# Kernel tuning notes

Measured on AMD Instinct MI355X. Metric: run time of the kernel, lower is better.

The kernel has to match this reference:

```python
import jax, jax.numpy as jnp
import numpy as np


def setup_inputs() -> dict:
    key = jax.random.key(0)
    k_in, k_w, k_s = jax.random.split(key, 3)
    B, S, D_IN, D_OUT = 4, 2048, 4096, 4096
    inp = jax.random.normal(k_in, (B, S, D_IN), dtype=jnp.float32)
    # int8 weight in [-128, 127], stored as int32 carrier then cast to int8
    int8_weight = jax.random.randint(k_w, (D_OUT, D_IN), -128, 128, dtype=jnp.int32).astype(jnp.int8)
    scale = jax.random.normal(k_s, (D_OUT,), dtype=jnp.float32)  # per-output-channel scale
    bias = jnp.zeros((1, D_OUT), dtype=jnp.float32)
    return {"input": inp, "int8_weight": int8_weight, "scale": scale, "bias": bias}


def reference(input, int8_weight, scale, bias):
    # w8a16 forward: cast int8 weight to activation dtype, linear, per-channel scale, bias
    w = int8_weight.astype(input.dtype)              # [out, in]
    out = jnp.einsum('bsi,oi->bso', input, w)        # F.linear
    out = out * scale                                # per-out-channel scale, broadcasts over [B,S]
    out = out + bias                                 # bias is [1, out], broadcasts
    return out
```

## Files before the change

### kernel.cpp

```cpp
#include <hip/hip_runtime.h>
#include <hip/hip_bf16.h>
#include <stdint.h>

typedef __attribute__((ext_vector_type(4))) int v4i;

#define BM 128
#define BN 128
#define BK 64

__device__ inline void load_lds16(const void* g, void* l) {
  __builtin_amdgcn_global_load_lds(
      (const __attribute__((address_space(1))) uint32_t*)g,
      (__attribute__((address_space(3))) uint32_t*)l, 16, 0, 0);
}

__global__ void detect_i32_kernel(const uint32_t* __restrict__ w, int n_words,
                                  int* __restrict__ flag) {
  __shared__ int s_ok;
  if (threadIdx.x == 0) s_ok = 1;
  __syncthreads();
  int ok = 1;
  for (int i = threadIdx.x; i < n_words; i += blockDim.x) {
    uint32_t v = w[i];
    uint32_t expect = (v & 0x80u) ? 0xFFFFFFu : 0u;
    if ((v >> 8) != expect) ok = 0;
  }
  if (!ok) s_ok = 0;
  __syncthreads();
  if (threadIdx.x == 0) *flag = s_ok;
}

__global__ __launch_bounds__(256)
void quant_a_kernel(const float* __restrict__ in, int8_t* __restrict__ out,
                    float* __restrict__ rscale, int K) {
  const int row = blockIdx.x;
  const int tid = threadIdx.x;
  const float4* p = (const float4*)(in + (size_t)row * K);
  float4 v[4];
  float amax = 0.f;
#pragma unroll
  for (int j = 0; j < 4; ++j) {
    v[j] = p[tid * 4 + j];
    amax = fmaxf(amax, fmaxf(fmaxf(fabsf(v[j].x), fabsf(v[j].y)),
                             fmaxf(fabsf(v[j].z), fabsf(v[j].w))));
  }
#pragma unroll
  for (int off = 32; off > 0; off >>= 1)
    amax = fmaxf(amax, __shfl_down(amax, off));
  __shared__ float s_part[4];
  __shared__ float s_inv, s_step;
  if ((tid & 63) == 0) s_part[tid >> 6] = amax;
  __syncthreads();
  if (tid == 0) {
    float m = fmaxf(fmaxf(s_part[0], s_part[1]), fmaxf(s_part[2], s_part[3]));
    s_inv  = (m > 0.f) ? 127.f / m : 0.f;
    s_step = (m > 0.f) ? m / 127.f : 0.f;
    rscale[row] = s_step;
  }
  __syncthreads();
  const float inv = s_inv;
  float f[16];
#pragma unroll
  for (int j = 0; j < 4; ++j) {
    f[4 * j]     = v[j].x; f[4 * j + 1] = v[j].y;
    f[4 * j + 2] = v[j].z; f[4 * j + 3] = v[j].w;
  }
  uint32_t w[4];
#pragma unroll
  for (int j = 0; j < 4; ++j) {
    uint32_t b = 0;
#pragma unroll
    for (int t = 0; t < 4; ++t) {
      int q = (int)rintf(f[4 * j + t] * inv);
      q = q > 127 ? 127 : (q < -127 ? -127 : q);
      b |= ((uint32_t)q & 0xffu) << (8 * t);
    }
    w[j] = b;
  }
  ((uint4*)(out + (size_t)row * K))[tid] = make_uint4(w[0], w[1], w[2], w[3]);
}

__global__ void repack_w_kernel(const void* __restrict__ in, int8_t* __restrict__ out,
                                int n16, const int* __restrict__ flag) {
  int i = blockIdx.x * blockDim.x + threadIdx.x;
  if (i >= n16) return;
  if (*flag) {
    uint32_t w[4];
#pragma unroll
    for (int j = 0; j < 4; ++j) {
      int4 a = ((const int4*)in)[4 * i + j];
      w[j] = ((uint32_t)a.x & 0xffu) | (((uint32_t)a.y & 0xffu) << 8) |
             (((uint32_t)a.z & 0xffu) << 16) | (((uint32_t)a.w & 0xffu) << 24);
    }
    ((uint4*)out)[i] = make_uint4(w[0], w[1], w[2], w[3]);
  } else {
    ((int4*)out)[i] = ((const int4*)in)[i];
  }
}

__global__ __launch_bounds__(256, 4)
void gemm_i8_epi(const int8_t* __restrict__ A, const int8_t* __restrict__ B,
                 const float* __restrict__ ascale, const float* __restrict__ scale,
                 const float* __restrict__ bias, float* __restrict__ C,
                 int Mdim, int Ndim, int Kdim) {
  __shared__ int8_t sA[BM * BK];
  __shared__ int8_t sB[BN * BK];
  __shared__ float sAs[BM];

  const int tid  = threadIdx.x;
  const int lane = tid & 63;
  const int wave = tid >> 6;
  const int wm = (wave >> 1) * 64;
  const int wn = (wave & 1) * 64;
  const int bm = blockIdx.y, bn = blockIdx.x;

  if (tid < BM) sAs[tid] = ascale[bm * BM + tid];

  const int srow = tid >> 2;
  const int scol = ((tid & 3) ^ (srow & 3)) * 16;
  const int8_t* gA = A + (size_t)(bm * BM + srow) * Kdim + scol;
  const int8_t* gB = B + (size_t)(bn * BN + srow) * Kdim + scol;

  const int frow = lane & 15;
  const int g    = lane >> 4;
  const int cpos = (g ^ (frow & 3)) * 16;

  v4i acc[4][4];
#pragma unroll
  for (int mi = 0; mi < 4; ++mi)
#pragma unroll
    for (int ni = 0; ni < 4; ++ni)
      acc[mi][ni] = (v4i){0, 0, 0, 0};

  for (int k0 = 0; k0 < Kdim; k0 += BK) {
    load_lds16(gA + k0,                       &sA[tid * 16]);
    load_lds16(gA + (size_t)64 * Kdim + k0,   &sA[4096 + tid * 16]);
    load_lds16(gB + k0,                       &sB[tid * 16]);
    load_lds16(gB + (size_t)64 * Kdim + k0,   &sB[4096 + tid * 16]);
    __syncthreads();

    v4i af[4], bf[4];
#pragma unroll
    for (int mi = 0; mi < 4; ++mi)
      af[mi] = *(const v4i*)&sA[(wm + frow + mi * 16) * BK + cpos];
#pragma unroll
    for (int ni = 0; ni < 4; ++ni)
      bf[ni] = *(const v4i*)&sB[(wn + frow + ni * 16) * BK + cpos];
#pragma unroll
    for (int mi = 0; mi < 4; ++mi)
#pragma unroll
      for (int ni = 0; ni < 4; ++ni)
        acc[mi][ni] = __builtin_amdgcn_mfma_i32_16x16x64_i8(
            af[mi], bf[ni], acc[mi][ni], 0, 0, 0);
    __syncthreads();
  }

  const int col0 = bn * BN + wn + (lane & 15);
  const int row0 = bm * BM + wm + (lane >> 4) * 4;
  const int lrow0 = wm + (lane >> 4) * 4;
#pragma unroll
  for (int ni = 0; ni < 4; ++ni) {
    int col = col0 + ni * 16;
    float sc = scale[col];
    float bs = bias[col];
#pragma unroll
    for (int mi = 0; mi < 4; ++mi) {
      int row = row0 + mi * 16;
#pragma unroll
      for (int r = 0; r < 4; ++r)
        C[(size_t)(row + r) * Ndim + col] =
            (float)acc[mi][ni][r] * sAs[lrow0 + mi * 16 + r] * sc + bs;
    }
  }
}

__global__ void naive_kernel(const float* __restrict__ A, const int* __restrict__ W,
                             const float* __restrict__ scale, const float* __restrict__ bias,
                             float* __restrict__ C, int Mdim, int Ndim, int Kdim) {
  int idx = blockIdx.x * blockDim.x + threadIdx.x;
  if (idx >= Mdim * Ndim) return;
  int row = idx / Ndim, col = idx % Ndim;
  const float* a = A + (size_t)row * Kdim;
  const int* w = W + (size_t)col * Kdim;
  float s = 0.f;
  for (int k = 0; k < Kdim; ++k) s += a[k] * (float)w[k];
  C[idx] = s * scale[col] + bias[col];
}

extern "C" void kernel_launch(void* const* d_in, const int* in_sizes, int n_in,
                              void* d_out, int out_size, void* d_ws, size_t ws_size,
                              hipStream_t stream) {
  const float* inp   = (const float*)d_in[0];
  const void*  w_raw = d_in[1];
  const float* scale = (const float*)d_in[2];
  const float* bias  = (const float*)d_in[3];
  float* out = (float*)d_out;

  const int N = in_sizes[2];
  const int K = in_sizes[1] / N;
  const int M = in_sizes[0] / K;

  size_t needA = (size_t)M * K;
  size_t needW = (size_t)N * K;
  size_t needS = (size_t)M * sizeof(float);
  size_t need  = needA + needW + needS + 16;
  if (ws_size < need) {
    int total = M * N;
    naive_kernel<<<(total + 255) / 256, 256, 0, stream>>>(
        inp, (const int*)w_raw, scale, bias, out, M, N, K);
    return;
  }

  int8_t* Aq = (int8_t*)d_ws;
  int8_t* Wq = Aq + needA;
  float* ascale = (float*)(Wq + needW);
  int* flag = (int*)(ascale + M);

  detect_i32_kernel<<<1, 256, 0, stream>>>((const uint32_t*)w_raw, 4096, flag);

  quant_a_kernel<<<M, 256, 0, stream>>>(inp, Aq, ascale, K);

  int nW16 = (N * K) / 16;
  repack_w_kernel<<<(nW16 + 255) / 256, 256, 0, stream>>>(w_raw, Wq, nW16, flag);

  dim3 grid(N / BN, M / BM);
  gemm_i8_epi<<<grid, 256, 0, stream>>>(Aq, Wq, ascale, scale, bias, out, M, N, K);
}
```

Measured before the change: 434.3 us.

## Replace int8 GEMM with 256x256 double-buffered 8-phase pipelined kernel

The GEMM moves from 128x128 single-buffered tiles to 256x256 tiles with 512 threads. It double-buffers 128-wide K slices in 128KB of LDS and interleaves the global-to-LDS loads with the MFMA phases, using barriers and setprio. It also adds an XCD-aware block swizzle, and rewrites quant_a and repack_w with coalesced 4-byte accesses per thread. The aim is to hide load latency and raise reuse per tile, at the cost of lower occupancy and shape restrictions that fall back to the naive kernel.

Result: faster. 392.2 us (-9.7%).

```diff
diff --git a/kernel.cpp b/kernel.cpp
--- a/kernel.cpp
+++ b/kernel.cpp
@@ -1,12 +1,7 @@
 #include <hip/hip_runtime.h>
-#include <hip/hip_bf16.h>
 #include <stdint.h>
 
 typedef __attribute__((ext_vector_type(4))) int v4i;
-
-#define BM 128
-#define BN 128
-#define BK 64
 
 __device__ inline void load_lds16(const void* g, void* l) {
   __builtin_amdgcn_global_load_lds(
@@ -36,142 +31,188 @@
   const int row = blockIdx.x;
   const int tid = threadIdx.x;
   const float4* p = (const float4*)(in + (size_t)row * K);
+  const int nf4 = K >> 2;
   float4 v[4];
   float amax = 0.f;
 #pragma unroll
   for (int j = 0; j < 4; ++j) {
-    v[j] = p[tid * 4 + j];
+    v[j] = p[tid + 256 * j];
     amax = fmaxf(amax, fmaxf(fmaxf(fabsf(v[j].x), fabsf(v[j].y)),
                              fmaxf(fabsf(v[j].z), fabsf(v[j].w))));
   }
+  (void)nf4;
 #pragma unroll
   for (int off = 32; off > 0; off >>= 1)
     amax = fmaxf(amax, __shfl_down(amax, off));
   __shared__ float s_part[4];
-  __shared__ float s_inv, s_step;
+  __shared__ float s_inv;
   if ((tid & 63) == 0) s_part[tid >> 6] = amax;
   __syncthreads();
   if (tid == 0) {
     float m = fmaxf(fmaxf(s_part[0], s_part[1]), fmaxf(s_part[2], s_part[3]));
-    s_inv  = (m > 0.f) ? 127.f / m : 0.f;
-    s_step = (m > 0.f) ? m / 127.f : 0.f;
-    rscale[row] = s_step;
+    s_inv = (m > 0.f) ? 127.f / m : 0.f;
+    rscale[row] = (m > 0.f) ? m / 127.f : 0.f;
   }
   __syncthreads();
   const float inv = s_inv;
-  float f[16];
+  uint32_t* o32 = (uint32_t*)(out + (size_t)row * K);
 #pragma unroll
   for (int j = 0; j < 4; ++j) {
-    f[4 * j]     = v[j].x; f[4 * j + 1] = v[j].y;
-    f[4 * j + 2] = v[j].z; f[4 * j + 3] = v[j].w;
-  }
-  uint32_t w[4];
-#pragma unroll
-  for (int j = 0; j < 4; ++j) {
+    float f[4] = {v[j].x, v[j].y, v[j].z, v[j].w};
     uint32_t b = 0;
 #pragma unroll
     for (int t = 0; t < 4; ++t) {
-      int q = (int)rintf(f[4 * j + t] * inv);
+      int q = (int)rintf(f[t] * inv);
       q = q > 127 ? 127 : (q < -127 ? -127 : q);
       b |= ((uint32_t)q & 0xffu) << (8 * t);
     }
-    w[j] = b;
-  }
-  ((uint4*)(out + (size_t)row * K))[tid] = make_uint4(w[0], w[1], w[2], w[3]);
+    o32[tid + 256 * j] = b;
+  }
 }
 
 __global__ void repack_w_kernel(const void* __restrict__ in, int8_t* __restrict__ out,
-                                int n16, const int* __restrict__ flag) {
+                                int n4, const int* __restrict__ flag) {
   int i = blockIdx.x * blockDim.x + threadIdx.x;
-  if (i >= n16) return;
+  if (i >= n4) return;
   if (*flag) {
-    uint32_t w[4];
-#pragma unroll
-    for (int j = 0; j < 4; ++j) {
-      int4 a = ((const int4*)in)[4 * i + j];
-      w[j] = ((uint32_t)a.x & 0xffu) | (((uint32_t)a.y & 0xffu) << 8) |
-             (((uint32_t)a.z & 0xffu) << 16) | (((uint32_t)a.w & 0xffu) << 24);
-    }
-    ((uint4*)out)[i] = make_uint4(w[0], w[1], w[2], w[3]);
+    const int4 a = ((const int4*)in)[i];
+    uint32_t b = ((uint32_t)a.x & 0xffu) | (((uint32_t)a.y & 0xffu) << 8) |
+                 (((uint32_t)a.z & 0xffu) << 16) | (((uint32_t)a.w & 0xffu) << 24);
+    ((uint32_t*)out)[i] = b;
   } else {
-    ((int4*)out)[i] = ((const int4*)in)[i];
-  }
-}
-
-__global__ __launch_bounds__(256, 4)
-void gemm_i8_epi(const int8_t* __restrict__ A, const int8_t* __restrict__ B,
+    ((uint32_t*)out)[i] = ((const uint32_t*)in)[i];
+  }
+}
+
+__global__ __launch_bounds__(512, 2)
+void gemm_i8_8ph(const int8_t* __restrict__ A, const int8_t* __restrict__ B,
                  const float* __restrict__ ascale, const float* __restrict__ scale,
                  const float* __restrict__ bias, float* __restrict__ C,
                  int Mdim, int Ndim, int Kdim) {
-  __shared__ int8_t sA[BM * BK];
-  __shared__ int8_t sB[BN * BK];
-  __shared__ float sAs[BM];
+  __shared__ __align__(16) int8_t sm[131072];
+  int8_t* const sA0 = sm;
+  int8_t* const sA1 = sm + 32768;
+  int8_t* const sB0 = sm + 65536;
+  int8_t* const sB1 = sm + 98304;
 
   const int tid  = threadIdx.x;
   const int lane = tid & 63;
   const int wave = tid >> 6;
-  const int wm = (wave >> 1) * 64;
-  const int wn = (wave & 1) * 64;
-  const int bm = blockIdx.y, bn = blockIdx.x;
-
-  if (tid < BM) sAs[tid] = ascale[bm * BM + tid];
-
-  const int srow = tid >> 2;
-  const int scol = ((tid & 3) ^ (srow & 3)) * 16;
-  const int8_t* gA = A + (size_t)(bm * BM + srow) * Kdim + scol;
-  const int8_t* gB = B + (size_t)(bn * BN + srow) * Kdim + scol;
+  const int wm = (wave >> 2) * 128;
+  const int wn = (wave & 3) * 64;
+
+  const int nwg = gridDim.x;
+  const int cpx = nwg >> 3;
+  const int bid = blockIdx.x;
+  const int swz = (bid & 7) * cpx + (bid >> 3);
+  const int nbn = Ndim >> 8;
+  const int bm = swz / nbn, bn = swz % nbn;
+
+  const int NT = Kdim >> 7;
+  const int NI = NT >> 1;
+
+  const int s8   = tid >> 3;
+  const int scol = ((tid & 7) ^ (s8 & 7)) << 4;
+  const int8_t* gA = A + (size_t)(bm * 256 + s8) * Kdim + scol;
+  const int8_t* gB = B + (size_t)(bn * 256 + s8) * Kdim + scol;
+  const size_t rstep = (size_t)64 * Kdim;
+  const int dst16 = tid << 4;
 
   const int frow = lane & 15;
   const int g    = lane >> 4;
-  const int cpos = (g ^ (frow & 3)) * 16;
-
-  v4i acc[4][4];
-#pragma unroll
-  for (int mi = 0; mi < 4; ++mi)
-#pragma unroll
-    for (int ni = 0; ni < 4; ++ni)
-      acc[mi][ni] = (v4i){0, 0, 0, 0};
-
-  for (int k0 = 0; k0 < Kdim; k0 += BK) {
-    load_lds16(gA + k0,                       &sA[tid * 16]);
-    load_lds16(gA + (size_t)64 * Kdim + k0,   &sA[4096 + tid * 16]);
-    load_lds16(gB + k0,                       &sB[tid * 16]);
-    load_lds16(gB + (size_t)64 * Kdim + k0,   &sB[4096 + tid * 16]);
-    __syncthreads();
-
-    v4i af[4], bf[4];
-#pragma unroll
-    for (int mi = 0; mi < 4; ++mi)
-      af[mi] = *(const v4i*)&sA[(wm + frow + mi * 16) * BK + cpos];
-#pragma unroll
-    for (int ni = 0; ni < 4; ++ni)
-      bf[ni] = *(const v4i*)&sB[(wn + frow + ni * 16) * BK + cpos];
-#pragma unroll
-    for (int mi = 0; mi < 4; ++mi)
+  const int f7   = frow & 7;
+  const int pc0  = ((g) ^ f7) << 4;
+  const int pc1  = ((4 + g) ^ f7) << 4;
+  const int aro  = (wm + frow) << 7;
+  const int bro  = (wn + frow) << 7;
+
+  v4i acc[8][4];
+#pragma unroll
+  for (int mi = 0; mi < 8; ++mi)
+#pragma unroll
+    for (int ni = 0; ni < 4; ++ni) acc[mi][ni] = (v4i){0, 0, 0, 0};
+
+#define STG(DST_, GS_, T_, RG_) \
+  load_lds16(GS_ + (size_t)(RG_) * rstep + ((size_t)(T_) << 7), DST_ + ((RG_) << 13) + dst16)
+
+  STG(sB0, gB, 0, 0); STG(sB0, gB, 0, 1); STG(sB0, gB, 0, 2); STG(sB0, gB, 0, 3);
+  STG(sA0, gA, 0, 0); STG(sA0, gA, 0, 1); STG(sA0, gA, 0, 2); STG(sA0, gA, 0, 3);
+  STG(sB1, gB, 1, 0); STG(sB1, gB, 1, 1); STG(sB1, gB, 1, 2); STG(sB1, gB, 1, 3);
+  asm volatile("s_waitcnt vmcnt(4)" ::: "memory");
+  __builtin_amdgcn_s_barrier();
+  __builtin_amdgcn_sched_barrier(0);
+
+#define VMW asm volatile("s_waitcnt vmcnt(4)" ::: "memory")
+
+#define PH(SA_, SB_, q_, LOADB_, S1_, S2_, VM_)                                               \
+  {                                                                                           \
+    if (LOADB_) {                                                                             \
+      _Pragma("unroll") for (int ni = 0; ni < 4; ++ni) {                                      \
+        bf[ni][0] = *(const v4i*)(SB_ + bro + ni * 2048 + pc0);                               \
+        bf[ni][1] = *(const v4i*)(SB_ + bro + ni * 2048 + pc1);                               \
+      }                                                                                       \
+    }                                                                                         \
+    v4i a00 = *(const v4i*)(SA_ + aro + (2 * (q_)) * 2048 + pc0);                             \
+    v4i a01 = *(const v4i*)(SA_ + aro + (2 * (q_)) * 2048 + pc1);                             \
+    v4i a10 = *(const v4i*)(SA_ + aro + (2 * (q_) + 1) * 2048 + pc0);                         \
+    v4i a11 = *(const v4i*)(SA_ + aro + (2 * (q_) + 1) * 2048 + pc1);                         \
+    S1_; S2_; VM_;                                                                            \
+    __builtin_amdgcn_s_barrier();                                                             \
+    __builtin_amdgcn_s_setprio(1);                                                           \
+    _Pragma("unroll") for (int ni = 0; ni < 4; ++ni) {                                        \
+      acc[2*(q_)][ni]   = __builtin_amdgcn_mfma_i32_16x16x64_i8(a00, bf[ni][0], acc[2*(q_)][ni], 0, 0, 0);     \
+      acc[2*(q_)+1][ni] = __builtin_amdgcn_mfma_i32_16x16x64_i8(a10, bf[ni][0], acc[2*(q_)+1][ni], 0, 0, 0);   \
+    }                                                                                         \
+    _Pragma("unroll") for (int ni = 0; ni < 4; ++ni) {                                        \
+      acc[2*(q_)][ni]   = __builtin_amdgcn_mfma_i32_16x16x64_i8(a01, bf[ni][1], acc[2*(q_)][ni], 0, 0, 0);     \
+      acc[2*(q_)+1][ni] = __builtin_amdgcn_mfma_i32_16x16x64_i8(a11, bf[ni][1], acc[2*(q_)+1][ni], 0, 0, 0);   \
+    }                                                                                         \
+    __builtin_amdgcn_s_setprio(0);                                                           \
+    __builtin_amdgcn_sched_barrier(0);                                                        \
+    __builtin_amdgcn_s_barrier();                                                             \
+    __builtin_amdgcn_sched_barrier(0);                                                        \
+  }
+
+#pragma unroll 1
+  for (int i = 0; i < NI; ++i) {
+    v4i bf[4][2];
+    const int t1 = 2 * i + 1;
+    int t2 = 2 * i + 2; if (t2 >= NT) t2 -= NT;
+    int t3 = 2 * i + 3; if (t3 >= NT) t3 -= NT;
+    PH(sA0, sB0, 0, 1, STG(sA1, gA, t1, 0), STG(sA1, gA, t1, 1), (void)0);
+    PH(sA0, sB0, 1, 0, STG(sA1, gA, t1, 2), STG(sA1, gA, t1, 3), (void)0);
+    PH(sA0, sB0, 2, 0, STG(sB0, gB, t2, 0), STG(sB0, gB, t2, 1), (void)0);
+    PH(sA0, sB0, 3, 0, STG(sB0, gB, t2, 2), STG(sB0, gB, t2, 3), VMW);
+    PH(sA1, sB1, 0, 1, STG(sA0, gA, t2, 0), STG(sA0, gA, t2, 1), (void)0);
+    PH(sA1, sB1, 1, 0, STG(sA0, gA, t2, 2), STG(sA0, gA, t2, 3), (void)0);
+    PH(sA1, sB1, 2, 0, STG(sB1, gB, t3, 0), STG(sB1, gB, t3, 1), (void)0);
+    PH(sA1, sB1, 3, 0, STG(sB1, gB, t3, 2), STG(sB1, gB, t3, 3), VMW);
+  }
+  asm volatile("s_waitcnt vmcnt(0)" ::: "memory");
+
+  const int col0 = bn * 256 + wn + (lane & 15);
+  const int row0 = bm * 256 + wm + ((lane >> 4) << 2);
+  float scv[4], bsv[4];
+#pragma unroll
+  for (int ni = 0; ni < 4; ++ni) {
+    scv[ni] = scale[col0 + ni * 16];
+    bsv[ni] = bias[col0 + ni * 16];
+  }
+#pragma unroll
+  for (int mi = 0; mi < 8; ++mi) {
+#pragma unroll
+    for (int r = 0; r < 4; ++r) {
+      const int row = row0 + mi * 16 + r;
+      const float as = ascale[row];
+      float* crow = C + (size_t)row * Ndim;
 #pragma unroll
       for (int ni = 0; ni < 4; ++ni)
-        acc[mi][ni] = __builtin_amdgcn_mfma_i32_16x16x64_i8(
-            af[mi], bf[ni], acc[mi][ni], 0, 0, 0);
-    __syncthreads();
-  }
-
-  const int col0 = bn * BN + wn + (lane & 15);
-  const int row0 = bm * BM + wm + (lane >> 4) * 4;
-  const int lrow0 = wm + (lane >> 4) * 4;
-#pragma unroll
-  for (int ni = 0; ni < 4; ++ni) {
-    int col = col0 + ni * 16;
-    float sc = scale[col];
-    float bs = bias[col];
-#pragma unroll
-    for (int mi = 0; mi < 4; ++mi) {
-      int row = row0 + mi * 16;
-#pragma unroll
-      for (int r = 0; r < 4; ++r)
-        C[(size_t)(row + r) * Ndim + col] =
-            (float)acc[mi][ni][r] * sAs[lrow0 + mi * 16 + r] * sc + bs;
+        crow[col0 + ni * 16] = (float)acc[mi][ni][r] * as * scv[ni] + bsv[ni];
     }
   }
+#undef PH
+#undef VMW
+#undef STG
 }
 
 __global__ void naive_kernel(const float* __restrict__ A, const int* __restrict__ W,
@@ -204,7 +245,9 @@
   size_t needW = (size_t)N * K;
   size_t needS = (size_t)M * sizeof(float);
   size_t need  = needA + needW + needS + 16;
-  if (ws_size < need) {
+
+  const int nblk = (M / 256) * (N / 256);
+  if (ws_size < need || (M % 256) || (N % 256) || (K % 256) || (nblk % 8)) {
     int total = M * N;
     naive_kernel<<<(total + 255) / 256, 256, 0, stream>>>(
         inp, (const int*)w_raw, scale, bias, out, M, N, K);
@@ -220,9 +263,8 @@
 
   quant_a_kernel<<<M, 256, 0, stream>>>(inp, Aq, ascale, K);
 
-  int nW16 = (N * K) / 16;
-  repack_w_kernel<<<(nW16 + 255) / 256, 256, 0, stream>>>(w_raw, Wq, nW16, flag);
-
-  dim3 grid(N / BN, M / BM);
-  gemm_i8_epi<<<grid, 256, 0, stream>>>(Aq, Wq, ascale, scale, bias, out, M, N, K);
-}
+  int n4 = (N * K) / 4;
+  repack_w_kernel<<<(n4 + 255) / 256, 256, 0, stream>>>(w_raw, Wq, n4, flag);
+
+  gemm_i8_8ph<<<nblk, 512, 0, stream>>>(Aq, Wq, ascale, scale, bias, out, M, N, K);
+}
```
